# Optimization experiments

Measured on AMD Instinct MI355X. Metric: run time of the kernel, lower is better.

The kernel has to match this reference:

```python
import jax, jax.numpy as jnp
import numpy as np

N_RAYS = 131072
N_SAMPLES = 128
BIG_DIST = 1e10  # sentinel last-interval distance, as in the torch code
EPS = 1e-10


def setup_inputs() -> dict:
    key = jax.random.key(0)
    k1, k2, k3 = jax.random.split(key, 3)
    raw = jax.random.normal(k1, (N_RAYS, N_SAMPLES, 4), dtype=jnp.float32)
    # integration depths must be sorted along the sample axis; typical near/far = [2, 6]
    z_vals = jnp.sort(
        jax.random.uniform(k2, (N_RAYS, N_SAMPLES), dtype=jnp.float32, minval=2.0, maxval=6.0),
        axis=-1,
    )
    rays_d = jax.random.normal(k3, (N_RAYS, 3), dtype=jnp.float32)
    return {"raw": raw, "z_vals": z_vals, "rays_d": rays_d}


def reference(raw, z_vals, rays_d):
    # distances between adjacent samples; last interval is 'infinite'
    dists = z_vals[..., 1:] - z_vals[..., :-1]                       # [R, S-1]
    dists = jnp.concatenate(
        [dists, jnp.full(dists[..., :1].shape, BIG_DIST, dists.dtype)], axis=-1
    )                                                                # [R, S]
    dists = dists * jnp.linalg.norm(rays_d, axis=-1, keepdims=True)  # scale by |d|

    rgb = jax.nn.sigmoid(raw[..., :3])                               # [R, S, 3]
    sigma = jax.nn.relu(raw[..., 3])                                 # raw_noise_std = 0
    alpha = 1.0 - jnp.exp(-sigma * dists)                            # [R, S]

    # exclusive cumprod of transmittance: T_i = prod_{j<i} (1 - alpha_j + eps)
    trans = jnp.cumprod(
        jnp.concatenate([jnp.ones_like(alpha[:, :1]), 1.0 - alpha + EPS], axis=-1),
        axis=-1,
    )[:, :-1]                                                        # [R, S]
    weights = alpha * trans                                          # [R, S]

    rgb_map = jnp.sum(weights[..., None] * rgb, axis=-2)             # [R, 3]
    depth_map = jnp.sum(weights * z_vals, axis=-1)                   # [R]
    acc_map = jnp.sum(weights, axis=-1)                              # [R]
    disp_map = 1.0 / jnp.maximum(EPS, depth_map / acc_map)           # [R]
    # white_bkgd = False, so no background compositing
    return rgb_map, disp_map, acc_map, weights, depth_map
```

## Files before the change

kernel.cpp:

```cpp
#include <hip/hip_runtime.h>
#include <math.h>

#define N_RAYS    131072
#define N_SAMPLES 128
#define BIG_DIST  1e10f
#define EPS       1e-10f

#define OFF_RGB    0
#define OFF_DISP   393216
#define OFF_ACC    524288
#define OFF_W      655360
#define OFF_DEPTH  17432576

__global__ __launch_bounds__(256) void nerf_render_kernel(
    const float4* __restrict__ raw,
    const float*  __restrict__ z_vals,
    const float*  __restrict__ rays_d,
    float* __restrict__ out)
{
    const int r = blockIdx.x * blockDim.x + threadIdx.x;
    if (r >= N_RAYS) return;

    const float4* rawr = raw + (size_t)r * N_SAMPLES;
    const float4* zr4  = (const float4*)(z_vals + (size_t)r * N_SAMPLES);

    const float dx = rays_d[3 * r + 0];
    const float dy = rays_d[3 * r + 1];
    const float dz = rays_d[3 * r + 2];
    const float nrm = sqrtf(dx * dx + dy * dy + dz * dz);

    float T = 1.0f;
    float cr = 0.f, cg = 0.f, cb = 0.f;
    float depth = 0.f, acc = 0.f;

    float* wout = out + OFF_W + (size_t)r * N_SAMPLES;

    float4 z0 = zr4[0];
    float4 z1 = zr4[1];

    for (int c = 0; c < N_SAMPLES / 8; ++c) {
        const int s0 = c * 8;

        float4 rv[8];
#pragma unroll
        for (int j = 0; j < 8; ++j) rv[j] = rawr[s0 + j];

        float zarr[9];
        zarr[0] = z0.x; zarr[1] = z0.y; zarr[2] = z0.z; zarr[3] = z0.w;
        zarr[4] = z1.x; zarr[5] = z1.y; zarr[6] = z1.z; zarr[7] = z1.w;

        float4 nz0, nz1;
        if (c < N_SAMPLES / 8 - 1) {
            nz0 = zr4[2 * c + 2];
            nz1 = zr4[2 * c + 3];
            zarr[8] = nz0.x;
        } else {
            nz0 = z0; nz1 = z1;
            zarr[8] = 0.0f;
        }

        float w8[8];
#pragma unroll
        for (int j = 0; j < 8; ++j) {
            const int s = s0 + j;
            float dist = (s == N_SAMPLES - 1) ? BIG_DIST : (zarr[j + 1] - zarr[j]);
            dist *= nrm;

            const float sigma = fmaxf(rv[j].w, 0.0f);
            const float alpha = 1.0f - __expf(-sigma * dist);
            const float w = alpha * T;
            T = T * (1.0f - alpha + EPS);

            const float sr = __builtin_amdgcn_rcpf(1.0f + __expf(-rv[j].x));
            const float sg = __builtin_amdgcn_rcpf(1.0f + __expf(-rv[j].y));
            const float sb = __builtin_amdgcn_rcpf(1.0f + __expf(-rv[j].z));

            cr += w * sr;
            cg += w * sg;
            cb += w * sb;
            depth += w * zarr[j];
            acc += w;
            w8[j] = w;
        }

        float4* w4 = (float4*)(wout + s0);
        w4[0] = make_float4(w8[0], w8[1], w8[2], w8[3]);
        w4[1] = make_float4(w8[4], w8[5], w8[6], w8[7]);

        z0 = nz0;
        z1 = nz1;
    }

    out[OFF_RGB + 3 * r + 0] = cr;
    out[OFF_RGB + 3 * r + 1] = cg;
    out[OFF_RGB + 3 * r + 2] = cb;
    out[OFF_ACC + r] = acc;
    out[OFF_DEPTH + r] = depth;
    out[OFF_DISP + r] = 1.0f / fmaxf(EPS, depth / acc);
}

extern "C" void kernel_launch(void* const* d_in, const int* in_sizes, int n_in,
                              void* d_out, int out_size, void* d_ws, size_t ws_size,
                              hipStream_t stream) {
    const float4* raw    = (const float4*)d_in[0];
    const float*  z_vals = (const float*)d_in[1];
    const float*  rays_d = (const float*)d_in[2];
    float* out = (float*)d_out;

    const int block = 256;
    const int grid  = (N_RAYS + block - 1) / block;
    nerf_render_kernel<<<grid, block, 0, stream>>>(raw, z_vals, rays_d, out);
}
```

Measured before the change: 476.6 us.

## Map one wavefront per ray with shuffle-based transmittance scan

```diff
diff --git a/kernel.cpp b/kernel.cpp
--- a/kernel.cpp
+++ b/kernel.cpp
@@ -12,91 +12,89 @@
 #define OFF_W      655360
 #define OFF_DEPTH  17432576
 
-__global__ __launch_bounds__(256) void nerf_render_kernel(
+__global__ __launch_bounds__(256) void nerf_render_scan_kernel(
     const float4* __restrict__ raw,
     const float*  __restrict__ z_vals,
     const float*  __restrict__ rays_d,
     float* __restrict__ out)
 {
-    const int r = blockIdx.x * blockDim.x + threadIdx.x;
+    const int tid  = blockIdx.x * blockDim.x + threadIdx.x;
+    const int r    = tid >> 6;
+    const int lane = threadIdx.x & 63;
     if (r >= N_RAYS) return;
 
     const float4* rawr = raw + (size_t)r * N_SAMPLES;
-    const float4* zr4  = (const float4*)(z_vals + (size_t)r * N_SAMPLES);
+    const float4  rv0 = rawr[2 * lane];
+    const float4  rv1 = rawr[2 * lane + 1];
 
-    const float dx = rays_d[3 * r + 0];
-    const float dy = rays_d[3 * r + 1];
-    const float dz = rays_d[3 * r + 2];
-    const float nrm = sqrtf(dx * dx + dy * dy + dz * dz);
+    const float2* zr2 = (const float2*)(z_vals + (size_t)r * N_SAMPLES);
+    const float2  z   = zr2[lane];
 
-    float T = 1.0f;
-    float cr = 0.f, cg = 0.f, cb = 0.f;
-    float depth = 0.f, acc = 0.f;
+    const float znext = __shfl_down(z.x, 1);
 
-    float* wout = out + OFF_W + (size_t)r * N_SAMPLES;
+    const float dxx = rays_d[3 * r + 0];
+    const float dyy = rays_d[3 * r + 1];
+    const float dzz = rays_d[3 * r + 2];
+    const float nrm = sqrtf(dxx * dxx + dyy * dyy + dzz * dzz);
 
-    float4 z0 = zr4[0];
-    float4 z1 = zr4[1];
+    const float dist0 = (z.y - z.x) * nrm;
+    const float dist1 = (lane == 63) ? (BIG_DIST * nrm) : ((znext - z.y) * nrm);
 
-    for (int c = 0; c < N_SAMPLES / 8; ++c) {
-        const int s0 = c * 8;
+    const float sig0 = fmaxf(rv0.w, 0.0f);
+    const float sig1 = fmaxf(rv1.w, 0.0f);
+    const float a0 = 1.0f - __expf(-sig0 * dist0);
+    const float a1 = 1.0f - __expf(-sig1 * dist1);
 
-        float4 rv[8];
+    const float f0 = 1.0f - a0 + EPS;
+    const float f1 = 1.0f - a1 + EPS;
+    const float p  = f0 * f1;
+
+    float sp = p;
 #pragma unroll
-        for (int j = 0; j < 8; ++j) rv[j] = rawr[s0 + j];
+    for (int off = 1; off < 64; off <<= 1) {
+        const float t = __shfl_up(sp, off);
+        sp *= (lane >= off) ? t : 1.0f;
+    }
+    float Texc = __shfl_up(sp, 1);
+    if (lane == 0) Texc = 1.0f;
 
-        float zarr[9];
-        zarr[0] = z0.x; zarr[1] = z0.y; zarr[2] = z0.z; zarr[3] = z0.w;
-        zarr[4] = z1.x; zarr[5] = z1.y; zarr[6] = z1.z; zarr[7] = z1.w;
+    const float T0 = Texc;
+    const float T1 = Texc * f0;
+    const float w0 = a0 * T0;
+    const float w1 = a1 * T1;
 
-        float4 nz0, nz1;
-        if (c < N_SAMPLES / 8 - 1) {
-            nz0 = zr4[2 * c + 2];
-            nz1 = zr4[2 * c + 3];
-            zarr[8] = nz0.x;
-        } else {
-            nz0 = z0; nz1 = z1;
-            zarr[8] = 0.0f;
-        }
+    ((float2*)(out + OFF_W + (size_t)r * N_SAMPLES))[lane] = make_float2(w0, w1);
 
-        float w8[8];
+    const float sr0 = __builtin_amdgcn_rcpf(1.0f + __expf(-rv0.x));
+    const float sg0 = __builtin_amdgcn_rcpf(1.0f + __expf(-rv0.y));
+    const float sb0 = __builtin_amdgcn_rcpf(1.0f + __expf(-rv0.z));
+    const float sr1 = __builtin_amdgcn_rcpf(1.0f + __expf(-rv1.x));
+    const float sg1 = __builtin_amdgcn_rcpf(1.0f + __expf(-rv1.y));
+    const float sb1 = __builtin_amdgcn_rcpf(1.0f + __expf(-rv1.z));
+
+    float cr    = w0 * sr0 + w1 * sr1;
+    float cg    = w0 * sg0 + w1 * sg1;
+    float cb    = w0 * sb0 + w1 * sb1;
+    float depth = w0 * z.x + w1 * z.y;
+    float acc   = w0 + w1;
+
 #pragma unroll
-        for (int j = 0; j < 8; ++j) {
-            const int s = s0 + j;
-            float dist = (s == N_SAMPLES - 1) ? BIG_DIST : (zarr[j + 1] - zarr[j]);
-            dist *= nrm;
-
-            const float sigma = fmaxf(rv[j].w, 0.0f);
-            const float alpha = 1.0f - __expf(-sigma * dist);
-            const float w = alpha * T;
-            T = T * (1.0f - alpha + EPS);
-
-            const float sr = __builtin_amdgcn_rcpf(1.0f + __expf(-rv[j].x));
-            const float sg = __builtin_amdgcn_rcpf(1.0f + __expf(-rv[j].y));
-            const float sb = __builtin_amdgcn_rcpf(1.0f + __expf(-rv[j].z));
-
-            cr += w * sr;
-            cg += w * sg;
-            cb += w * sb;
-            depth += w * zarr[j];
-            acc += w;
-            w8[j] = w;
-        }
-
-        float4* w4 = (float4*)(wout + s0);
-        w4[0] = make_float4(w8[0], w8[1], w8[2], w8[3]);
-        w4[1] = make_float4(w8[4], w8[5], w8[6], w8[7]);
-
-        z0 = nz0;
-        z1 = nz1;
+    for (int m = 32; m > 0; m >>= 1) {
+        cr    += __shfl_xor(cr, m);
+        cg    += __shfl_xor(cg, m);
+        cb    += __shfl_xor(cb, m);
+        depth += __shfl_xor(depth, m);
+        acc   += __shfl_xor(acc, m);
     }
 
-    out[OFF_RGB + 3 * r + 0] = cr;
-    out[OFF_RGB + 3 * r + 1] = cg;
-    out[OFF_RGB + 3 * r + 2] = cb;
-    out[OFF_ACC + r] = acc;
-    out[OFF_DEPTH + r] = depth;
-    out[OFF_DISP + r] = 1.0f / fmaxf(EPS, depth / acc);
+    if (lane == 0) {
+        out[OFF_RGB + 3 * r + 0] = cr;
+        out[OFF_RGB + 3 * r + 1] = cg;
+        out[OFF_RGB + 3 * r + 2] = cb;
+        out[OFF_ACC + r]   = acc;
+        out[OFF_DEPTH + r] = depth;
+        out[OFF_DISP + r]  = 1.0f / fmaxf(EPS, depth / acc);
+    }
 }
 
 extern "C" void kernel_launch(void* const* d_in, const int* in_sizes, int n_in,
@@ -108,6 +106,7 @@
     float* out = (float*)d_out;
 
     const int block = 256;
-    const int grid  = (N_RAYS + block - 1) / block;
-    nerf_render_kernel<<<grid, block, 0, stream>>>(raw, z_vals, rays_d, out);
+    const int rays_per_block = block / 64;
+    const int grid = N_RAYS / rays_per_block;
+    nerf_render_scan_kernel<<<grid, block, 0, stream>>>(raw, z_vals, rays_d, out);
 }
```

Result: faster. 410.1 us (-14.0%).
